# Kernel tuning notes

Measured on AMD Instinct MI355X. Metric: run time of the kernel, lower is better.

The kernel has to match this reference:

```python
import jax, jax.numpy as jnp
import numpy as np

CH = 512
GROUPS = 32  # _valid_num_groups(512, 32)
EPS = 1e-6

def setup_inputs() -> dict:
    key = jax.random.key(0)
    ks = jax.random.split(key, 11)
    B, C, H, W = 8, CH, 64, 64
    s = 0.02
    return {
        "x": jax.random.normal(ks[0], (B, C, H, W), jnp.float32),
        "gn_w": jnp.ones((C,), jnp.float32),
        "gn_b": jnp.zeros((C,), jnp.float32),
        "q_w": jax.random.normal(ks[1], (C, C), jnp.float32) * s,
        "q_b": jnp.zeros((C,), jnp.float32),
        "k_w": jax.random.normal(ks[2], (C, C), jnp.float32) * s,
        "k_b": jnp.zeros((C,), jnp.float32),
        "v_w": jax.random.normal(ks[3], (C, C), jnp.float32) * s,
        "v_b": jnp.zeros((C,), jnp.float32),
        "proj_w": jax.random.normal(ks[4], (C, C), jnp.float32) * s,
        "proj_b": jnp.zeros((C,), jnp.float32),
    }

def _group_norm(x, w, b):
    B, C, H, W = x.shape
    g = GROUPS
    xg = x.reshape(B, g, C // g, H, W)
    mu = xg.mean(axis=(2, 3, 4), keepdims=True)
    var = xg.var(axis=(2, 3, 4), keepdims=True)
    xn = ((xg - mu) * jax.lax.rsqrt(var + EPS)).reshape(B, C, H, W)
    return xn * w[None, :, None, None] + b[None, :, None, None]

def _conv1x1(h, w, b):
    # h: [B,C,H,W]; w: [Cout,Cin]; 1x1 conv == channel matmul
    return jnp.einsum('bchw,dc->bdhw', h, w) + b[None, :, None, None]

def reference(x, gn_w, gn_b, q_w, q_b, k_w, k_b, v_w, v_b, proj_w, proj_b):
    B, C, H, W = x.shape
    N = H * W
    h = _group_norm(x, gn_w, gn_b)
    q = _conv1x1(h, q_w, q_b).reshape(B, C, N)  # [B,C,N]
    k = _conv1x1(h, k_w, k_b).reshape(B, C, N)
    v = _conv1x1(h, v_w, v_b).reshape(B, C, N)
    # attn[b,i,j] = sum_c q[b,c,i]*k[b,c,j] scaled
    attn = jnp.einsum('bci,bcj->bij', q, k) * (C ** -0.5)
    attn = jax.nn.softmax(attn, axis=-1)
    # out[b,c,i] = sum_j v[b,c,j]*attn[b,i,j]  (bmm(v, attn^T))
    o = jnp.einsum('bcj,bij->bci', v, attn).reshape(B, C, H, W)
    o = _conv1x1(o, proj_w, proj_b)
    return x + o
```

## Files before the change

kernel.cpp:

```cpp
#include <hip/hip_runtime.h>

typedef unsigned short u16;
typedef __attribute__((ext_vector_type(8))) short short8;
typedef __attribute__((ext_vector_type(4))) float f32x4;

__device__ __forceinline__ u16 f32_to_bf16(float f) {
  unsigned u = __float_as_uint(f);
  u += 0x7fffu + ((u >> 16) & 1u);
  return (u16)(u >> 16);
}
__device__ __forceinline__ float bf16_to_f32(u16 h) {
  return __uint_as_float(((unsigned)h) << 16);
}

#define GLD_LDS16(gp, lp)                                                  \
  __builtin_amdgcn_global_load_lds(                                        \
      (const __attribute__((address_space(1))) void*)(gp),                 \
      (__attribute__((address_space(3))) void*)(lp), 16, 0, 0)

__global__ __launch_bounds__(256) void cvt4_f32_bf16(const float* __restrict__ s0,
                                                     const float* __restrict__ s1,
                                                     const float* __restrict__ s2,
                                                     const float* __restrict__ s3,
                                                     u16* __restrict__ d0,
                                                     u16* __restrict__ d1,
                                                     u16* __restrict__ d2,
                                                     u16* __restrict__ d3) {
  const float* s = blockIdx.y == 0 ? s0 : blockIdx.y == 1 ? s1 : blockIdx.y == 2 ? s2 : s3;
  u16* d = blockIdx.y == 0 ? d0 : blockIdx.y == 1 ? d1 : blockIdx.y == 2 ? d2 : d3;
  int i = blockIdx.x * 256 + threadIdx.x;
  float4 v = ((const float4*)s)[i];
  uint2 r;
  r.x = (unsigned)f32_to_bf16(v.x) | ((unsigned)f32_to_bf16(v.y) << 16);
  r.y = (unsigned)f32_to_bf16(v.z) | ((unsigned)f32_to_bf16(v.w) << 16);
  ((uint2*)d)[i] = r;
}

__global__ __launch_bounds__(1024) void gn_stats(const float* __restrict__ x,
                                                 float2* __restrict__ stats) {
  int bg = blockIdx.x;
  const float* xp = x + (long)bg * 65536;
  int t = threadIdx.x;
  float s = 0.f, ss = 0.f;
  for (int i = t; i < 16384; i += 1024) {
    float4 v = ((const float4*)xp)[i];
    s += (v.x + v.y) + (v.z + v.w);
    ss += (v.x * v.x + v.y * v.y) + (v.z * v.z + v.w * v.w);
  }
#pragma unroll
  for (int o = 32; o; o >>= 1) { s += __shfl_xor(s, o); ss += __shfl_xor(ss, o); }
  __shared__ float rs[16], rq[16];
  int wave = t >> 6, lane = t & 63;
  if (lane == 0) { rs[wave] = s; rq[wave] = ss; }
  __syncthreads();
  if (wave == 0) {
    float a = lane < 16 ? rs[lane] : 0.f;
    float b = lane < 16 ? rq[lane] : 0.f;
#pragma unroll
    for (int o = 8; o; o >>= 1) { a += __shfl_xor(a, o); b += __shfl_xor(b, o); }
    if (lane == 0) {
      float mean = a * (1.f / 65536.f);
      float var = b * (1.f / 65536.f) - mean * mean;
      stats[bg] = make_float2(mean, rsqrtf(var + 1e-6f));
    }
  }
}

__global__ __launch_bounds__(256) void gn_apply_t(const float* __restrict__ x,
                                                  const float* __restrict__ gw,
                                                  const float* __restrict__ gb,
                                                  const float2* __restrict__ stats,
                                                  u16* __restrict__ hT) {
  const int g = blockIdx.y, bb = blockIdx.z;
  const float2 st = stats[bb * 32 + g];
  const float mean = st.x, rstd = st.y;
  const float* xp = x + ((long)bb * 512 + g * 16) * 4096;
  u16* hp = hT + (long)bb * 4096 * 512 + g * 16;
  const int i = blockIdx.x * 1024 + threadIdx.x * 4;
#pragma unroll
  for (int half = 0; half < 2; ++half) {
    float w[8], bv[8];
#pragma unroll
    for (int c = 0; c < 8; ++c) {
      w[c] = gw[g * 16 + half * 8 + c] * rstd;
      bv[c] = gb[g * 16 + half * 8 + c];
    }
    float v[8][4];
#pragma unroll
    for (int c = 0; c < 8; ++c) {
      float4 f = *(const float4*)(xp + (long)(half * 8 + c) * 4096 + i);
      v[c][0] = f.x; v[c][1] = f.y; v[c][2] = f.z; v[c][3] = f.w;
    }
#pragma unroll
    for (int p = 0; p < 4; ++p) {
      u16 o[8];
#pragma unroll
      for (int c = 0; c < 8; ++c) o[c] = f32_to_bf16((v[c][p] - mean) * w[c] + bv[c]);
      *(int4*)(hp + (long)(i + p) * 512 + half * 8) = *(int4*)o;
    }
  }
}

template <int EPI>
__global__ __launch_bounds__(256) void gemm128(
    const u16* __restrict__ Ab, long sA, int lda,
    const u16* __restrict__ Bb, long sB, int ldb,
    void* __restrict__ Cb, long sC, int ldc,
    const float* __restrict__ biasM, const float* __restrict__ biasN,
    float scale, const float* __restrict__ res, long sR, int K) {
  const u16* A = Ab + (long)blockIdx.z * sA;
  const u16* B = Bb + (long)blockIdx.z * sB;
  const int m0 = blockIdx.y * 128, n0 = blockIdx.x * 128;
  const int t = threadIdx.x;
  const int wave = t >> 6, lane = t & 63;
  const int wy = wave >> 1, wx = wave & 1;
  const int lr = lane & 15, q = lane >> 4;
  __shared__ __align__(16) u16 As[128 * 32];
  __shared__ __align__(16) u16 Bs[128 * 32];
  f32x4 acc[4][4] = {};
  for (int k0 = 0; k0 < K; k0 += 32) {
#pragma unroll
    for (int c = 0; c < 2; ++c) {
      const int chunk = c * 256 + t;
      const int row = chunk >> 2, ko = (chunk & 3) << 3;
      const int ldsoff = (c * 256 + wave * 64) * 8;
      GLD_LDS16(A + (long)(m0 + row) * lda + (k0 + ko), As + ldsoff);
      GLD_LDS16(B + (long)(n0 + row) * ldb + (k0 + ko), Bs + ldsoff);
    }
    __syncthreads();
    short8 af[4], bf[4];
#pragma unroll
    for (int i = 0; i < 4; ++i)
      af[i] = *(const short8*)(&As[(wy * 64 + i * 16 + lr) * 32 + q * 8]);
#pragma unroll
    for (int j = 0; j < 4; ++j)
      bf[j] = *(const short8*)(&Bs[(wx * 64 + j * 16 + lr) * 32 + q * 8]);
#pragma unroll
    for (int i = 0; i < 4; ++i)
#pragma unroll
      for (int j = 0; j < 4; ++j)
        acc[i][j] = __builtin_amdgcn_mfma_f32_16x16x32_bf16(af[i], bf[j], acc[i][j], 0, 0, 0);
    __syncthreads();
  }
#pragma unroll
  for (int i = 0; i < 4; ++i) {
#pragma unroll
    for (int r = 0; r < 4; ++r) {
      const int mr = m0 + wy * 64 + i * 16 + q * 4 + r;
      const float bm = biasM ? biasM[mr] : 0.f;
#pragma unroll
      for (int j = 0; j < 4; ++j) {
        const int nc = n0 + wx * 64 + j * 16 + lr;
        float vv = acc[i][j][r] + bm;
        if (biasN) vv += biasN[nc];
        vv *= scale;
        const long off = (long)blockIdx.z * sC + (long)mr * ldc + nc;
        if (EPI == 0) {
          ((u16*)Cb)[off] = f32_to_bf16(vv);
        } else {
          ((float*)Cb)[off] = vv + res[(long)blockIdx.z * sR + (long)mr * ldc + nc];
        }
      }
    }
  }
}

__global__ __launch_bounds__(256) void softmax_kernel(u16* __restrict__ P) {
  u16* pr = P + (long)blockIdx.y * 4096 * 4096 + (long)blockIdx.x * 4096;
  int t = threadIdx.x;
  int lane = t & 63, wave = t >> 6;
  int4 d0 = ((const int4*)pr)[t];
  int4 d1 = ((const int4*)pr)[t + 256];
  const u16* p0 = (const u16*)&d0;
  const u16* p1 = (const u16*)&d1;
  float v[16];
#pragma unroll
  for (int j = 0; j < 8; ++j) { v[j] = bf16_to_f32(p0[j]); v[8 + j] = bf16_to_f32(p1[j]); }
  float mx = v[0];
#pragma unroll
  for (int j = 1; j < 16; ++j) mx = fmaxf(mx, v[j]);
#pragma unroll
  for (int o = 32; o; o >>= 1) mx = fmaxf(mx, __shfl_xor(mx, o));
  __shared__ float sm[4];
  __shared__ float ssum[4];
  if (lane == 0) sm[wave] = mx;
  __syncthreads();
  mx = fmaxf(fmaxf(sm[0], sm[1]), fmaxf(sm[2], sm[3]));
  float s = 0.f;
#pragma unroll
  for (int j = 0; j < 16; ++j) { v[j] = __expf(v[j] - mx); s += v[j]; }
#pragma unroll
  for (int o = 32; o; o >>= 1) s += __shfl_xor(s, o);
  if (lane == 0) ssum[wave] = s;
  __syncthreads();
  s = ssum[0] + ssum[1] + ssum[2] + ssum[3];
  float inv = 1.0f / s;
  unsigned r0[4], r1[4];
#pragma unroll
  for (int j = 0; j < 4; ++j) {
    r0[j] = (unsigned)f32_to_bf16(v[2 * j] * inv) | ((unsigned)f32_to_bf16(v[2 * j + 1] * inv) << 16);
    r1[j] = (unsigned)f32_to_bf16(v[8 + 2 * j] * inv) | ((unsigned)f32_to_bf16(v[8 + 2 * j + 1] * inv) << 16);
  }
  ((int4*)pr)[t] = *(int4*)r0;
  ((int4*)pr)[t + 256] = *(int4*)r1;
}

extern "C" void kernel_launch(void* const* d_in, const int* in_sizes, int n_in,
                              void* d_out, int out_size, void* d_ws, size_t ws_size,
                              hipStream_t stream) {
  const float* x = (const float*)d_in[0];
  const float* gn_w = (const float*)d_in[1];
  const float* gn_b = (const float*)d_in[2];
  const float* q_w = (const float*)d_in[3];
  const float* q_b = (const float*)d_in[4];
  const float* k_w = (const float*)d_in[5];
  const float* k_b = (const float*)d_in[6];
  const float* v_w = (const float*)d_in[7];
  const float* v_b = (const float*)d_in[8];
  const float* p_w = (const float*)d_in[9];
  const float* p_b = (const float*)d_in[10];

  char* ws = (char*)d_ws;
  const size_t MB = 1ull << 20;
  u16* wqb = (u16*)(ws + 0);
  u16* wkb = (u16*)(ws + 512 * 1024);
  u16* wvb = (u16*)(ws + 1 * MB);
  u16* wpb = (u16*)(ws + 3 * MB / 2);
  u16* hb = (u16*)(ws + 2 * MB);
  u16* vb = (u16*)(ws + 34 * MB);
  u16* Pb = (u16*)(ws + 66 * MB);
  float2* stats = (float2*)(ws + 66 * MB);
  u16* qb = (u16*)d_out;
  u16* kb = (u16*)d_out + 512L * 4096 * 8;
  u16* ob = hb;

  int NB = 1;
  if (ws_size >= 66 * MB + 8 * 32 * MB) NB = 8;
  else if (ws_size >= 66 * MB + 4 * 32 * MB) NB = 4;
  else if (ws_size >= 66 * MB + 2 * 32 * MB) NB = 2;

  cvt4_f32_bf16<<<dim3(256, 4), 256, 0, stream>>>(q_w, k_w, v_w, p_w, wqb, wkb, wvb, wpb);
  gn_stats<<<256, 1024, 0, stream>>>(x, stats);
  gn_apply_t<<<dim3(4, 32, 8), 256, 0, stream>>>(x, gn_w, gn_b, stats, hb);

  const long sCN = 512L * 4096;
  const long sNN = 4096L * 4096;
  const float scale = 0.04419417382415922f;

  gemm128<0><<<dim3(4, 32, 8), 256, 0, stream>>>(
      hb, sCN, 512, wqb, 0, 512, qb, sCN, 512, nullptr, q_b, scale, nullptr, 0, 512);
  gemm128<0><<<dim3(4, 32, 8), 256, 0, stream>>>(
      hb, sCN, 512, wkb, 0, 512, kb, sCN, 512, nullptr, k_b, 1.0f, nullptr, 0, 512);
  gemm128<0><<<dim3(32, 4, 8), 256, 0, stream>>>(
      wvb, 0, 512, hb, sCN, 512, vb, sCN, 4096, v_b, nullptr, 1.0f, nullptr, 0, 512);

  for (int b0 = 0; b0 < 8; b0 += NB) {
    gemm128<0><<<dim3(32, 32, NB), 256, 0, stream>>>(
        qb + b0 * sCN, sCN, 512, kb + b0 * sCN, sCN, 512, Pb, sNN, 4096,
        nullptr, nullptr, 1.0f, nullptr, 0, 512);
    softmax_kernel<<<dim3(4096, NB), 256, 0, stream>>>(Pb);
    gemm128<0><<<dim3(4, 32, NB), 256, 0, stream>>>(
        Pb, sNN, 4096, vb + b0 * sCN, sCN, 4096, ob + b0 * sCN, sCN, 512,
        nullptr, nullptr, 1.0f, nullptr, 0, 4096);
  }

  gemm128<1><<<dim3(32, 4, 8), 256, 0, stream>>>(
      wpb, 0, 512, ob, sCN, 512, (float*)d_out, sCN, 4096, p_b, nullptr, 1.0f,
      x, sCN, 512);
}
```

Measured before the change: 968.9 us.

## Add 256-row, 512-thread bf16 GEMM with 4-stage LDS pipeline for QKV/attention

```diff
diff --git a/kernel.cpp b/kernel.cpp
--- a/kernel.cpp
+++ b/kernel.cpp
@@ -17,6 +17,14 @@
   __builtin_amdgcn_global_load_lds(                                        \
       (const __attribute__((address_space(1))) void*)(gp),                 \
       (__attribute__((address_space(3))) void*)(lp), 16, 0, 0)
+
+#define WAITVM(n) asm volatile("s_waitcnt vmcnt(" #n ")" ::: "memory")
+
+__device__ __forceinline__ void wg_barrier() {
+  asm volatile("" ::: "memory");
+  __builtin_amdgcn_s_barrier();
+  asm volatile("" ::: "memory");
+}
 
 __global__ __launch_bounds__(256) void cvt4_f32_bf16(const float* __restrict__ s0,
                                                      const float* __restrict__ s1,
@@ -97,6 +105,132 @@
 #pragma unroll
       for (int c = 0; c < 8; ++c) o[c] = f32_to_bf16((v[c][p] - mean) * w[c] + bv[c]);
       *(int4*)(hp + (long)(i + p) * 512 + half * 8) = *(int4*)o;
+    }
+  }
+}
+
+template <int BN>
+__global__ __launch_bounds__(512, 2) void gemm256(
+    const u16* __restrict__ Ab, long sA, int lda,
+    const u16* __restrict__ Bb, long sB, int ldb,
+    u16* __restrict__ Cb, long sC, int ldc,
+    const float* __restrict__ biasM, const float* __restrict__ biasN,
+    float scale, int K) {
+  constexpr int NFR = BN / 64;
+  constexpr int BCH = (BN * 32 * 2) / (512 * 16);
+  __shared__ __align__(16) u16 As[4][256 * 32];
+  __shared__ __align__(16) u16 Bs[4][BN * 32];
+  const u16* A = Ab + (long)blockIdx.z * sA;
+  const u16* B = Bb + (long)blockIdx.z * sB;
+  const int m0 = blockIdx.y * 256, n0 = blockIdx.x * BN;
+  const int t = threadIdx.x;
+  const int wave = t >> 6, lane = t & 63;
+  const int wy = wave >> 2, wx = wave & 3;
+  const int lr = lane & 15, q = lane >> 4;
+  const int NT = K >> 5;
+
+  long aoff[2];
+  int aldsb[2];
+#pragma unroll
+  for (int cc = 0; cc < 2; ++cc) {
+    int c = cc * 512 + t;
+    int row = c >> 2, sl = c & 3;
+    int qs = sl ^ ((row >> 1) & 3);
+    aoff[cc] = (long)(m0 + row) * lda + qs * 8;
+    aldsb[cc] = (cc * 512 + wave * 64) * 8;
+  }
+  long boff[BCH];
+  int bldsb[BCH];
+#pragma unroll
+  for (int cc = 0; cc < BCH; ++cc) {
+    int c = cc * 512 + t;
+    int row = c >> 2, sl = c & 3;
+    int qs = sl ^ ((row >> 1) & 3);
+    boff[cc] = (long)(n0 + row) * ldb + qs * 8;
+    bldsb[cc] = (cc * 512 + wave * 64) * 8;
+  }
+
+  auto stageA = [&](int tt2) {
+    const int bi2 = tt2 & 3;
+    const long kk = (long)tt2 << 5;
+#pragma unroll
+    for (int cc = 0; cc < 2; ++cc) GLD_LDS16(A + aoff[cc] + kk, &As[bi2][aldsb[cc]]);
+  };
+  auto stageB = [&](int tt2) {
+    const int bi2 = tt2 & 3;
+    const long kk = (long)tt2 << 5;
+#pragma unroll
+    for (int cc = 0; cc < BCH; ++cc) GLD_LDS16(B + boff[cc] + kk, &Bs[bi2][bldsb[cc]]);
+  };
+
+  const int so = ((q ^ ((lr >> 1) & 3)) << 3);
+  const int arow = wy * 128;
+  const int brow = wx * (BN / 4);
+
+  f32x4 acc[8][NFR] = {};
+
+  stageA(0); stageB(0); stageA(1); stageB(1); stageA(2); stageB(2);
+
+  for (int tt = 0; tt < NT; ++tt) {
+    const int bi = tt & 3;
+    if (tt + 3 < NT) stageA(tt + 3);
+    const int nf = NT - 1 - tt;
+    if (BN == 256) {
+      if (nf >= 3) WAITVM(10);
+      else if (nf == 2) WAITVM(8);
+      else if (nf == 1) WAITVM(4);
+      else WAITVM(0);
+    } else {
+      if (nf >= 3) WAITVM(8);
+      else if (nf == 2) WAITVM(6);
+      else if (nf == 1) WAITVM(3);
+      else WAITVM(0);
+    }
+    wg_barrier();
+    short8 a0[4], bfr[NFR];
+#pragma unroll
+    for (int i = 0; i < 4; ++i)
+      a0[i] = *(const short8*)(&As[bi][0] + (arow + i * 16 + lr) * 32 + so);
+#pragma unroll
+    for (int j = 0; j < NFR; ++j)
+      bfr[j] = *(const short8*)(&Bs[bi][0] + (brow + j * 16 + lr) * 32 + so);
+    __builtin_amdgcn_s_setprio(1);
+#pragma unroll
+    for (int i = 0; i < 4; ++i)
+#pragma unroll
+      for (int j = 0; j < NFR; ++j)
+        acc[i][j] = __builtin_amdgcn_mfma_f32_16x16x32_bf16(a0[i], bfr[j], acc[i][j], 0, 0, 0);
+    __builtin_amdgcn_s_setprio(0);
+    wg_barrier();
+    if (tt + 3 < NT) stageB(tt + 3);
+    short8 a1[4];
+#pragma unroll
+    for (int i = 0; i < 4; ++i)
+      a1[i] = *(const short8*)(&As[bi][0] + (arow + 64 + i * 16 + lr) * 32 + so);
+    __builtin_amdgcn_s_setprio(1);
+#pragma unroll
+    for (int i = 0; i < 4; ++i)
+#pragma unroll
+      for (int j = 0; j < NFR; ++j)
+        acc[4 + i][j] = __builtin_amdgcn_mfma_f32_16x16x32_bf16(a1[i], bfr[j], acc[4 + i][j], 0, 0, 0);
+    __builtin_amdgcn_s_setprio(0);
+    wg_barrier();
+  }
+
+#pragma unroll
+  for (int i = 0; i < 8; ++i) {
+#pragma unroll
+    for (int r = 0; r < 4; ++r) {
+      const int mr = m0 + wy * 128 + i * 16 + q * 4 + r;
+      const float bm = biasM ? biasM[mr] : 0.f;
+#pragma unroll
+      for (int j = 0; j < NFR; ++j) {
+        const int nc = n0 + wx * (BN / 4) + j * 16 + lr;
+        float vv = acc[i][j][r] + bm;
+        if (biasN) vv += biasN[nc];
+        vv *= scale;
+        Cb[(long)blockIdx.z * sC + (long)mr * ldc + nc] = f32_to_bf16(vv);
+      }
     }
   }
 }
@@ -247,21 +381,21 @@
   const long sNN = 4096L * 4096;
   const float scale = 0.04419417382415922f;
 
-  gemm128<0><<<dim3(4, 32, 8), 256, 0, stream>>>(
-      hb, sCN, 512, wqb, 0, 512, qb, sCN, 512, nullptr, q_b, scale, nullptr, 0, 512);
-  gemm128<0><<<dim3(4, 32, 8), 256, 0, stream>>>(
-      hb, sCN, 512, wkb, 0, 512, kb, sCN, 512, nullptr, k_b, 1.0f, nullptr, 0, 512);
-  gemm128<0><<<dim3(32, 4, 8), 256, 0, stream>>>(
-      wvb, 0, 512, hb, sCN, 512, vb, sCN, 4096, v_b, nullptr, 1.0f, nullptr, 0, 512);
+  gemm256<256><<<dim3(2, 16, 8), 512, 0, stream>>>(
+      hb, sCN, 512, wqb, 0, 512, qb, sCN, 512, nullptr, q_b, scale, 512);
+  gemm256<256><<<dim3(2, 16, 8), 512, 0, stream>>>(
+      hb, sCN, 512, wkb, 0, 512, kb, sCN, 512, nullptr, k_b, 1.0f, 512);
+  gemm256<256><<<dim3(16, 2, 8), 512, 0, stream>>>(
+      wvb, 0, 512, hb, sCN, 512, vb, sCN, 4096, v_b, nullptr, 1.0f, 512);
 
   for (int b0 = 0; b0 < 8; b0 += NB) {
-    gemm128<0><<<dim3(32, 32, NB), 256, 0, stream>>>(
+    gemm256<256><<<dim3(16, 16, NB), 512, 0, stream>>>(
         qb + b0 * sCN, sCN, 512, kb + b0 * sCN, sCN, 512, Pb, sNN, 4096,
-        nullptr, nullptr, 1.0f, nullptr, 0, 512);
+        nullptr, nullptr, 1.0f, 512);
     softmax_kernel<<<dim3(4096, NB), 256, 0, stream>>>(Pb);
-    gemm128<0><<<dim3(4, 32, NB), 256, 0, stream>>>(
+    gemm256<128><<<dim3(4, 16, NB), 512, 0, stream>>>(
         Pb, sNN, 4096, vb + b0 * sCN, sCN, 4096, ob + b0 * sCN, sCN, 512,
-        nullptr, nullptr, 1.0f, nullptr, 0, 4096);
+        nullptr, nullptr, 1.0f, 4096);
   }
 
   gemm128<1><<<dim3(32, 4, 8), 256, 0, stream>>>(
```

New measurement: 968.3 us. Within noise of the previous version (-0.1%).
